# Kernel optimization log

Measured on AMD Instinct MI355X. Metric: run time of the kernel, lower is better.

## Reference

```python
import jax, jax.numpy as jnp
import numpy as np

T = 4          # spiking time steps
TAU = 2.0      # LIF leak
ALPHA = 4.0    # surrogate sigmoid sharpness
EPS = 1e-5     # batchnorm eps
HEADS = 12
SCALE = 0.125

@jax.custom_vjp
def spike(x):
    return (x >= 0).astype(x.dtype)

def _spike_fwd(x):
    return (x >= 0).astype(x.dtype), x

def _spike_bwd(x, g):
    s = jax.nn.sigmoid(ALPHA * x)
    return (g * ALPHA * s * (1.0 - s),)

spike.defvjp(_spike_fwd, _spike_bwd)

def lif(x, threshold):
    # x: (T*B, ...). layer_by_layer LIF: scan membrane over time axis.
    xt = x.reshape((T, -1) + x.shape[1:])
    def step(mem, xi):
        mem = mem + (xi - mem) / TAU
        s = spike(mem - threshold)
        mem = mem * (1.0 - jax.lax.stop_gradient(s))  # hard reset, detached
        return mem, s
    _, spikes = jax.lax.scan(step, jnp.zeros_like(xt[0]), xt)
    return spikes.reshape(x.shape)

def bn(x, gamma, beta):
    # training-mode batchnorm over all axes except channel axis 1
    axes = (0,) + tuple(range(2, x.ndim))
    mean = x.mean(axes, keepdims=True)
    var = x.var(axes, keepdims=True)
    shp = (1, -1) + (1,) * (x.ndim - 2)
    return (x - mean) * jax.lax.rsqrt(var + EPS) * gamma.reshape(shp) + beta.reshape(shp)

def forward(x, q_w, q_gamma, q_beta, k_w, k_gamma, k_beta, v_w, v_gamma, v_beta,
            proj_w, proj_b, proj_gamma, proj_beta,
            fc1_w, fc1_b, bn1_gamma, bn1_beta, fc2_w, fc2_b, bn2_gamma, bn2_beta):
    TB, C, H, W = x.shape
    N = H * W
    dh = C // HEADS
    xf = x.reshape(TB, C, N)

    def qkv_branch(w, g, b):
        y = lif(bn(jnp.einsum('oc,bcn->bon', w, xf), g, b), 1.0)  # (TB,C,N)
        # (TB,C,N) -> (TB,N,C) -> (TB,N,h,d) -> (TB,h,N,d)
        return y.transpose(0, 2, 1).reshape(TB, N, HEADS, dh).transpose(0, 2, 1, 3)

    q = qkv_branch(q_w, q_gamma, q_beta)
    k = qkv_branch(k_w, k_gamma, k_beta)
    v = qkv_branch(v_w, v_gamma, v_beta)

    kv = jnp.einsum('bhnd,bhne->bhde', k, v)          # (TB,h,d,d)
    attn = jnp.einsum('bhnd,bhde->bhne', q, kv) * SCALE  # (TB,h,N,d)
    attn = attn.transpose(0, 1, 3, 2)                 # (TB,h,d,N)
    attn = lif(attn, 0.5).reshape(TB, C, N)

    proj = jnp.einsum('oc,bcn->bon', proj_w, attn) + proj_b[None, :, None]
    proj = lif(bn(proj, proj_gamma, proj_beta), 1.0).reshape(TB, C, H, W)
    x = x + proj

    h1 = jnp.einsum('oc,bchw->bohw', fc1_w, x) + fc1_b.reshape(1, -1, 1, 1)
    h1 = lif(bn(h1, bn1_gamma, bn1_beta), 1.0)
    h2 = jnp.einsum('oc,bchw->bohw', fc2_w, h1) + fc2_b.reshape(1, -1, 1, 1)
    h2 = lif(bn(h2, bn2_gamma, bn2_beta), 1.0)
    return x + h2

def setup_inputs():
    key = jax.random.key(0)
    B, C, H, W = 32, 384, 14, 14
    Hd = 4 * C
    ks = jax.random.split(key, 8)
    sC = 1.0 / np.sqrt(C)
    sH = 1.0 / np.sqrt(Hd)
    return {
        'x': jax.random.normal(ks[0], (T * B, C, H, W), jnp.float32),
        'q_w': jax.random.normal(ks[1], (C, C), jnp.float32) * sC,
        'q_gamma': jnp.ones((C,), jnp.float32), 'q_beta': jnp.zeros((C,), jnp.float32),
        'k_w': jax.random.normal(ks[2], (C, C), jnp.float32) * sC,
        'k_gamma': jnp.ones((C,), jnp.float32), 'k_beta': jnp.zeros((C,), jnp.float32),
        'v_w': jax.random.normal(ks[3], (C, C), jnp.float32) * sC,
        'v_gamma': jnp.ones((C,), jnp.float32), 'v_beta': jnp.zeros((C,), jnp.float32),
        'proj_w': jax.random.normal(ks[4], (C, C), jnp.float32) * sC,
        'proj_b': jnp.zeros((C,), jnp.float32),
        'proj_gamma': jnp.ones((C,), jnp.float32), 'proj_beta': jnp.zeros((C,), jnp.float32),
        'fc1_w': jax.random.normal(ks[5], (Hd, C), jnp.float32) * sC,
        'fc1_b': jnp.zeros((Hd,), jnp.float32),
        'bn1_gamma': jnp.ones((Hd,), jnp.float32), 'bn1_beta': jnp.zeros((Hd,), jnp.float32),
        'fc2_w': jax.random.normal(ks[6], (C, Hd), jnp.float32) * sH,
        'fc2_b': jnp.zeros((C,), jnp.float32),
        'bn2_gamma': jnp.ones((C,), jnp.float32), 'bn2_beta': jnp.zeros((C,), jnp.float32),
    }

def reference(x, q_w, q_gamma, q_beta, k_w, k_gamma, k_beta, v_w, v_gamma, v_beta,
              proj_w, proj_b, proj_gamma, proj_beta,
              fc1_w, fc1_b, bn1_gamma, bn1_beta, fc2_w, fc2_b, bn2_gamma, bn2_beta):
    return forward(x, q_w, q_gamma, q_beta, k_w, k_gamma, k_beta, v_w, v_gamma, v_beta,
                   proj_w, proj_b, proj_gamma, proj_beta,
                   fc1_w, fc1_b, bn1_gamma, bn1_beta, fc2_w, fc2_b, bn2_gamma, bn2_beta)
```

## Files before the change

kernel.cpp:

```cpp
#include <hip/hip_runtime.h>
#include <stdint.h>

#define NBN   25088
#define NTOK  196
#define BATCH 32
#define CDIM  384
#define HDIM  1536
#define NHEAD 12

typedef float f32x4 __attribute__((ext_vector_type(4)));

#define GLDS16(g, l) __builtin_amdgcn_global_load_lds( \
    (const __attribute__((address_space(1))) void*)(g), \
    (__attribute__((address_space(3))) void*)(l), 16, 0, 0)

__global__ __launch_bounds__(256) void k_transpose(const float* __restrict__ x,
                                                   float* __restrict__ xT) {
  int id = blockIdx.x * 256 + threadIdx.x;
  int c = id / NBN;
  int r = id - c * NBN;
  int b = r / NTOK;
  int n = r - b * NTOK;
  xT[id] = x[((size_t)b * CDIM + c) * NTOK + n];
}

__global__ __launch_bounds__(256) void k_wT(const float* __restrict__ src,
                                            float* __restrict__ dst,
                                            int C, int ldd, int coff) {
  __shared__ float t[32][33];
  const int c0 = blockIdx.x * 32, r0 = blockIdx.y * 32;
  const int tx = threadIdx.x & 31, ty = threadIdx.x >> 5;
#pragma unroll
  for (int i = 0; i < 4; ++i)
    t[ty + i * 8][tx] = src[(size_t)(r0 + ty + i * 8) * C + c0 + tx];
  __syncthreads();
#pragma unroll
  for (int i = 0; i < 4; ++i)
    dst[(size_t)(c0 + ty + i * 8) * ldd + coff + r0 + tx] = t[tx][ty + i * 8];
}

template <typename TIN, int MT>
__global__ __launch_bounds__(256, 3) void k_gemm10(
    const float* __restrict__ WT, const TIN* __restrict__ X,
    const float* __restrict__ bias, float* __restrict__ Y,
    double* __restrict__ pS, double* __restrict__ pS2, int K, int Mtot) {
  __shared__ float As[32][MT];
  __shared__ float Bs[32][128];
  constexpr int MR = MT / 16;
  const int tid = threadIdx.x;
  const int lane = tid & 63, wv = tid >> 6;
  const int gy = blockIdx.x, bn = blockIdx.y;
  const int wcol = gy * MT;
  const int tx = tid & 15, ty = tid >> 4;
  const int NK = K >> 5;

  float acc[MR][8];
#pragma unroll
  for (int i = 0; i < MR; ++i)
#pragma unroll
    for (int j = 0; j < 8; ++j) acc[i][j] = 0.f;

  for (int ks = 0; ks < NK; ++ks) {
    const int k0 = ks << 5;
    __syncthreads();
    if constexpr (MT == 128) {
      const int lrow = wv * 2 + (lane >> 5), lcol = (lane & 31) * 4;
#pragma unroll
      for (int i = 0; i < 4; ++i)
        GLDS16(WT + (size_t)(k0 + i * 8 + lrow) * Mtot + wcol + lcol,
               &As[i * 8 + wv * 2][0]);
    } else {
      const int lrow = wv * 4 + (lane >> 4), lcol = (lane & 15) * 4;
#pragma unroll
      for (int i = 0; i < 2; ++i)
        GLDS16(WT + (size_t)(k0 + i * 16 + lrow) * Mtot + wcol + lcol,
               &As[i * 16 + wv * 4][0]);
    }
    if constexpr (__is_same(TIN, float)) {
      const int lrow = wv * 2 + (lane >> 5), lcol = (lane & 31) * 4;
#pragma unroll
      for (int i = 0; i < 4; ++i)
        GLDS16(X + (size_t)(k0 + i * 8 + lrow) * NBN + bn * 128 + lcol,
               &Bs[i * 8 + wv * 2][0]);
    } else {
      const int r = tid >> 3, c16 = tid & 7;
      const uint4 d = *reinterpret_cast<const uint4*>(
          &X[(size_t)(k0 + r) * NBN + bn * 128 + c16 * 16]);
      const uint32_t wd[4] = {d.x, d.y, d.z, d.w};
#pragma unroll
      for (int q = 0; q < 4; ++q) {
        f32x4 f;
        f[0] = (float)(wd[q] & 0xffu);
        f[1] = (float)((wd[q] >> 8) & 0xffu);
        f[2] = (float)((wd[q] >> 16) & 0xffu);
        f[3] = (float)(wd[q] >> 24);
        *reinterpret_cast<f32x4*>(&Bs[r][c16 * 16 + q * 4]) = f;
      }
    }
    asm volatile("s_waitcnt vmcnt(0)" ::: "memory");
    __syncthreads();

    auto lA0 = [&](int kk) { return *reinterpret_cast<const f32x4*>(&As[kk][ty * 4]); };
    auto lA1 = [&](int kk) { return *reinterpret_cast<const f32x4*>(&As[kk][64 + ty * 4]); };
    auto lB0 = [&](int kk) { return *reinterpret_cast<const f32x4*>(&Bs[kk][tx * 4]); };
    auto lB1 = [&](int kk) { return *reinterpret_cast<const f32x4*>(&Bs[kk][64 + tx * 4]); };
    auto FMA = [&](f32x4 a0, f32x4 a1, f32x4 b0, f32x4 b1) {
#pragma unroll
      for (int i = 0; i < MR; ++i) {
        const float av = (i < 4) ? a0[i] : a1[i - 4];
#pragma unroll
        for (int j = 0; j < 8; ++j) {
          const float bv = (j < 4) ? b0[j] : b1[j - 4];
          acc[i][j] = fmaf(av, bv, acc[i][j]);
        }
      }
    };
    f32x4 xa0, xa1, xb0, xb1, ya0, ya1, yb0, yb1;
    xa0 = lA0(0);
    if constexpr (MT == 128) xa1 = lA1(0);
    xb0 = lB0(0);
    xb1 = lB1(0);
#pragma unroll
    for (int kk = 0; kk < 32; kk += 2) {
      ya0 = lA0(kk + 1);
      if constexpr (MT == 128) ya1 = lA1(kk + 1);
      yb0 = lB0(kk + 1);
      yb1 = lB1(kk + 1);
      FMA(xa0, xa1, xb0, xb1);
      if (kk + 2 < 32) {
        xa0 = lA0(kk + 2);
        if constexpr (MT == 128) xa1 = lA1(kk + 2);
        xb0 = lB0(kk + 2);
        xb1 = lB1(kk + 2);
      }
      FMA(ya0, ya1, yb0, yb1);
    }
  }

#pragma unroll
  for (int i = 0; i < MR; ++i) {
    const int rl = (MT == 128) ? ((i < 4) ? (ty * 4 + i) : (64 + ty * 4 + i - 4))
                               : (ty * 4 + i);
    const int row = wcol + rl;
    const float bv = bias ? bias[row] : 0.f;
    float4 o0, o1;
    o0.x = acc[i][0] + bv; o0.y = acc[i][1] + bv;
    o0.z = acc[i][2] + bv; o0.w = acc[i][3] + bv;
    o1.x = acc[i][4] + bv; o1.y = acc[i][5] + bv;
    o1.z = acc[i][6] + bv; o1.w = acc[i][7] + bv;
    *reinterpret_cast<float4*>(&Y[(size_t)row * NBN + bn * 128 + tx * 4]) = o0;
    *reinterpret_cast<float4*>(&Y[(size_t)row * NBN + bn * 128 + 64 + tx * 4]) = o1;
    double s = (double)o0.x + (double)o0.y + (double)o0.z + (double)o0.w +
               (double)o1.x + (double)o1.y + (double)o1.z + (double)o1.w;
    double s2 = (double)o0.x * o0.x + (double)o0.y * o0.y + (double)o0.z * o0.z +
                (double)o0.w * o0.w + (double)o1.x * o1.x + (double)o1.y * o1.y +
                (double)o1.z * o1.z + (double)o1.w * o1.w;
#pragma unroll
    for (int off = 1; off < 16; off <<= 1) {
      s += __shfl_xor(s, off, 64);
      s2 += __shfl_xor(s2, off, 64);
    }
    if (tx == 0) {
      pS[(size_t)bn * Mtot + row] = s;
      pS2[(size_t)bn * Mtot + row] = s2;
    }
  }
}

__global__ __launch_bounds__(256) void k_repack(const uint8_t* __restrict__ sp,
                                                uint32_t* __restrict__ bitsT) {
  __shared__ uint32_t bb[64][48];
  const int col0 = blockIdx.x * 64;
  const int c = threadIdx.x & 63, q = threadIdx.x >> 6;
#pragma unroll
  for (int wi = 0; wi < 12; ++wi) {
    const int w = q * 12 + wi;
    uint32_t word = 0;
#pragma unroll
    for (int j = 0; j < 32; ++j)
      word |= (uint32_t)(sp[(size_t)(32 * w + j) * NBN + col0 + c] & 1) << j;
    bb[c][w] = word;
  }
  __syncthreads();
  for (int i = threadIdx.x; i < 64 * 48; i += 256)
    bitsT[(size_t)col0 * 48 + i] = bb[i / 48][i % 48];
}

__global__ __launch_bounds__(256) void k_spgemm(
    const uint32_t* __restrict__ bitsT, const float* __restrict__ WT,
    const float* __restrict__ bias, float* __restrict__ Y,
    double* __restrict__ pS, double* __restrict__ pS2) {
  __shared__ float ytile[4][384];
  const int tid = threadIdx.x;
  const int lane = tid & 63, wv = tid >> 6;
  const int c = blockIdx.x * 4 + wv;
  const uint32_t* wb = bitsT + (size_t)c * 48;

  float a0 = 0.f, a1 = 0.f, a2 = 0.f, a3 = 0.f, a4 = 0.f, a5 = 0.f;
  for (int w = 0; w < 48; ++w) {
    uint32_t word = wb[w];
    while (word) {
      const int k = w * 32 + __builtin_ctz(word);
      word &= word - 1;
      const float* wr = WT + (size_t)k * 384;
      a0 += wr[lane];
      a1 += wr[64 + lane];
      a2 += wr[128 + lane];
      a3 += wr[192 + lane];
      a4 += wr[256 + lane];
      a5 += wr[320 + lane];
    }
  }
  ytile[wv][lane]       = a0 + bias[lane];
  ytile[wv][64 + lane]  = a1 + bias[64 + lane];
  ytile[wv][128 + lane] = a2 + bias[128 + lane];
  ytile[wv][192 + lane] = a3 + bias[192 + lane];
  ytile[wv][256 + lane] = a4 + bias[256 + lane];
  ytile[wv][320 + lane] = a5 + bias[320 + lane];
  __syncthreads();
  const int c0 = blockIdx.x * 4;
  for (int r = tid; r < 384; r += 256) {
    float4 v;
    v.x = ytile[0][r]; v.y = ytile[1][r]; v.z = ytile[2][r]; v.w = ytile[3][r];
    *reinterpret_cast<float4*>(&Y[(size_t)r * NBN + c0]) = v;
    double s = (double)v.x + (double)v.y + (double)v.z + (double)v.w;
    double s2 = (double)v.x * v.x + (double)v.y * v.y + (double)v.z * v.z +
                (double)v.w * v.w;
    pS[(size_t)blockIdx.x * 384 + r] = s;
    pS2[(size_t)blockIdx.x * 384 + r] = s2;
  }
}

__global__ __launch_bounds__(64) void k_bn_reduceN(const double* __restrict__ pS,
                                                   const double* __restrict__ pS2,
                                                   float* __restrict__ mean,
                                                   float* __restrict__ rstd,
                                                   int Mtot, int NP) {
  const int ch = blockIdx.x, lane = threadIdx.x;
  double s = 0.0, s2 = 0.0;
  for (int j = lane; j < NP; j += 64) {
    s += pS[(size_t)j * Mtot + ch];
    s2 += pS2[(size_t)j * Mtot + ch];
  }
#pragma unroll
  for (int off = 32; off; off >>= 1) {
    s += __shfl_down(s, off, 64);
    s2 += __shfl_down(s2, off, 64);
  }
  if (lane == 0) {
    double m = s / (double)NBN;
    double v = s2 / (double)NBN - m * m;
    mean[ch] = (float)m;
    rstd[ch] = (float)(1.0 / sqrt(v + 1e-5));
  }
}

__global__ __launch_bounds__(256) void k_lif_pack(const float* __restrict__ Y,
    const float* __restrict__ mean, const float* __restrict__ rstd,
    const float* __restrict__ g0, const float* __restrict__ g1,
    const float* __restrict__ g2, const float* __restrict__ b0,
    const float* __restrict__ b1, const float* __restrict__ b2,
    uint32_t* __restrict__ pk) {
  const int o = blockIdx.x;
  const int b = threadIdx.x >> 3, w = threadIdx.x & 7;
  int br = o / 384, ol = o - br * 384;
  const float g = (br == 0 ? g0 : br == 1 ? g1 : g2)[ol];
  const float be = (br == 0 ? b0 : br == 1 ? b1 : b2)[ol];
  const float m_ = mean[o], rs_ = rstd[o];
  float mem[32];
#pragma unroll
  for (int j = 0; j < 32; ++j) mem[j] = 0.f;
  for (int t = 0; t < 4; ++t) {
    uint32_t word = 0;
    const size_t base = (size_t)o * NBN + (size_t)(t * 32 + b) * NTOK + w * 32;
#pragma unroll
    for (int q = 0; q < 8; ++q) {
      if (w * 32 + q * 4 < NTOK) {
        float4 v4 = *reinterpret_cast<const float4*>(&Y[base + q * 4]);
        float vv[4] = {v4.x, v4.y, v4.z, v4.w};
#pragma unroll
        for (int jj = 0; jj < 4; ++jj) {
          int j = q * 4 + jj;
          float v = ((vv[jj] - m_) * rs_) * g + be;
          float mm = mem[j];
          mm = mm + (v - mm) * 0.5f;
          bool fire = (mm >= 1.0f);
          mem[j] = fire ? 0.f : mm;
          word |= (fire ? 1u : 0u) << j;
        }
      }
    }
    pk[((size_t)o * 128 + t * 32 + b) * 8 + w] = word;
  }
}

__global__ __launch_bounds__(256) void k_lif_u8(const float* __restrict__ Y,
    const float* __restrict__ mean, const float* __restrict__ rstd,
    const float* __restrict__ gamma, const float* __restrict__ beta,
    uint8_t* __restrict__ sp) {
  const int o = blockIdx.x;
  const int b = threadIdx.x >> 3, w = threadIdx.x & 7;
  const float m_ = mean[o], rs_ = rstd[o], g = gamma[o], be = beta[o];
  float mem[32];
#pragma unroll
  for (int j = 0; j < 32; ++j) mem[j] = 0.f;
  for (int t = 0; t < 4; ++t) {
    const size_t base = (size_t)o * NBN + (size_t)(t * 32 + b) * NTOK + w * 32;
    uint32_t words[8];
#pragma unroll
    for (int q = 0; q < 8; ++q) {
      words[q] = 0;
      if (w * 32 + q * 4 < NTOK) {
        float4 v4 = *reinterpret_cast<const float4*>(&Y[base + q * 4]);
        float vv[4] = {v4.x, v4.y, v4.z, v4.w};
#pragma unroll
        for (int jj = 0; jj < 4; ++jj) {
          int j = q * 4 + jj;
          float v = ((vv[jj] - m_) * rs_) * g + be;
          float mm = mem[j];
          mm = mm + (v - mm) * 0.5f;
          bool fire = (mm >= 1.0f);
          mem[j] = fire ? 0.f : mm;
          words[q] |= (fire ? 1u : 0u) << (8 * jj);
        }
      }
    }
    uint32_t* dst = reinterpret_cast<uint32_t*>(const_cast<uint8_t*>(sp) + base);
#pragma unroll
    for (int q = 0; q < 8; ++q)
      if (w * 32 + q * 4 < NTOK) dst[q] = words[q];
  }
}

template <int MODE>
__global__ __launch_bounds__(256) void k_bn_lif(const float* __restrict__ Y,
                                                const float* __restrict__ mean,
                                                const float* __restrict__ rstd,
                                                const float* __restrict__ gamma,
                                                const float* __restrict__ beta,
                                                const float* __restrict__ addsrc,
                                                float* __restrict__ extra) {
  int id = blockIdx.x * 256 + threadIdx.x;
  int o = id / (BATCH * NTOK);
  int r = id - o * (BATCH * NTOK);
  float m_ = mean[o], rs_ = rstd[o], g = gamma[o], be = beta[o];
  float mem = 0.f;
#pragma unroll
  for (int t = 0; t < 4; ++t) {
    size_t idx = (size_t)o * NBN + (size_t)t * (BATCH * NTOK) + r;
    float v = Y[idx];
    v = ((v - m_) * rs_) * g + be;
    mem = mem + (v - mem) * 0.5f;
    bool fire = (mem >= 1.0f);
    float s = fire ? 1.f : 0.f;
    mem = fire ? 0.f : mem;
    if constexpr (MODE == 1) {
      extra[idx] = addsrc[idx] + s;
    } else {
      int b = r / NTOK, n = r - b * NTOK;
      extra[((size_t)(t * BATCH + b) * CDIM + o) * NTOK + n] = addsrc[idx] + s;
    }
  }
}

__global__ __launch_bounds__(256) void k_attn_pop(const uint32_t* __restrict__ pQ,
                                                  const uint32_t* __restrict__ pK,
                                                  const uint32_t* __restrict__ pV,
                                                  uint8_t* __restrict__ spA) {
  __shared__ __align__(16) uint32_t qw[32][8], kw[32][8], vw[32][8];
  __shared__ int kv[32][33];
  __shared__ uint32_t kvb[8][32];
  __shared__ uint32_t qT[NTOK];
  const int bh = blockIdx.x;
  const int b_ = bh / NHEAD, h = bh - b_ * NHEAD;
  const int tid = threadIdx.x;
  const int e = tid >> 3, w = tid & 7;
  float mem[32];
#pragma unroll
  for (int j = 0; j < 32; ++j) mem[j] = 0.f;

  for (int t = 0; t < 4; ++t) {
    const int tb = t * 32 + b_;
    {
      int d = tid >> 3, wo = tid & 7;
      size_t base = ((size_t)(h * 32 + d) * 128 + tb) * 8 + wo;
      qw[d][wo] = pQ[base];
      kw[d][wo] = pK[base];
      vw[d][wo] = pV[base];
    }
    __syncthreads();
    for (int i = tid; i < 1024; i += 256) {
      int d = i >> 5, ee = i & 31;
      const uint64_t* kp = reinterpret_cast<const uint64_t*>(&kw[d][0]);
      const uint64_t* vp = reinterpret_cast<const uint64_t*>(&vw[ee][0]);
      int s = 0;
#pragma unroll
      for (int u = 0; u < 4; ++u) s += __popcll(kp[u] & vp[u]);
      kv[d][ee] = s;
    }
    __syncthreads();
    {
      int bitb = tid >> 5, ee = tid & 31;
      uint32_t mword = 0;
#pragma unroll
      for (int d = 0; d < 32; ++d) mword |= (uint32_t)((kv[d][ee] >> bitb) & 1) << d;
      kvb[bitb][ee] = mword;
    }
    if (tid < NTOK) {
      uint32_t mword = 0;
#pragma unroll
      for (int d = 0; d < 32; ++d)
        mword |= ((qw[d][tid >> 5] >> (tid & 31)) & 1u) << d;
      qT[tid] = mword;
    }
    __syncthreads();
    uint32_t word = 0;
#pragma unroll
    for (int j = 0; j < 32; ++j) {
      int n = w * 32 + j;
      if (n < NTOK) {
        uint32_t qm = qT[n];
        int acc = 0;
#pragma unroll
        for (int bb = 0; bb < 8; ++bb) acc += __popc(qm & kvb[bb][e]) << bb;
        float val = (float)acc * 0.125f;
        float mm = mem[j];
        mm = mm + (val - mm) * 0.5f;
        bool fire = (mm >= 0.5f);
        mem[j] = fire ? 0.f : mm;
        word |= (fire ? 1u : 0u) << j;
      }
    }
    uint8_t* dst = spA + (size_t)(h * 32 + e) * NBN + (size_t)tb * NTOK + w * 32;
#pragma unroll
    for (int q = 0; q < 8; ++q) {
      if (w * 32 + q * 4 < NTOK) {
        uint32_t b4 = ((word >> (q * 4)) & 1u) | (((word >> (q * 4 + 1)) & 1u) << 8) |
                      (((word >> (q * 4 + 2)) & 1u) << 16) |
                      (((word >> (q * 4 + 3)) & 1u) << 24);
        *reinterpret_cast<uint32_t*>(dst + q * 4) = b4;
      }
    }
    __syncthreads();
  }
}

extern "C" void kernel_launch(void* const* d_in, const int* in_sizes, int n_in,
                              void* d_out, int out_size, void* d_ws, size_t ws_size,
                              hipStream_t stream) {
  const float* x          = (const float*)d_in[0];
  const float* q_w        = (const float*)d_in[1];
  const float* q_gamma    = (const float*)d_in[2];
  const float* q_beta     = (const float*)d_in[3];
  const float* k_w        = (const float*)d_in[4];
  const float* k_gamma    = (const float*)d_in[5];
  const float* k_beta     = (const float*)d_in[6];
  const float* v_w        = (const float*)d_in[7];
  const float* v_gamma    = (const float*)d_in[8];
  const float* v_beta     = (const float*)d_in[9];
  const float* proj_w     = (const float*)d_in[10];
  const float* proj_b     = (const float*)d_in[11];
  const float* proj_gamma = (const float*)d_in[12];
  const float* proj_beta  = (const float*)d_in[13];
  const float* fc1_w      = (const float*)d_in[14];
  const float* fc1_b      = (const float*)d_in[15];
  const float* bn1_gamma  = (const float*)d_in[16];
  const float* bn1_beta   = (const float*)d_in[17];
  const float* fc2_w      = (const float*)d_in[18];
  const float* fc2_b      = (const float*)d_in[19];
  const float* bn2_gamma  = (const float*)d_in[20];
  const float* bn2_beta   = (const float*)d_in[21];
  float* out = (float*)d_out;
  char* ws = (char*)d_ws;

  const size_t O_XT   = 0;
  const size_t O_YQ   = 38535168;
  const size_t O_XRES = 154140672;
  const size_t O_PK   = 192675840;
  const size_t O_SPA  = 197394432;
  const size_t O_H1SP = 192675840;
  const size_t O_H1   = 0;
  const size_t O_ST   = 231211008;
  const size_t O_P1   = 154140672;
  const size_t O_P1B  = O_P1 + 1806336;
  const size_t O_QKVT = 197394432;
  const size_t O_PRJT = 192675840;
  const size_t O_P2A  = 192675840;
  const size_t O_P2AB = O_P2A + 2408448;
  const size_t O_F1T  = 197492736;
  const size_t O_BT   = 0;
  const size_t O_F2T  = 4816896;
  const size_t O_P2B  = 77070336;
  const size_t O_P2BB = 96337920;

  float* xT    = (float*)(ws + O_XT);
  float* yQ    = (float*)(ws + O_YQ);
  float* yB    = (float*)(ws + O_YQ);
  float* h1    = (float*)(ws + O_H1);
  float* xres  = (float*)(ws + O_XRES);
  uint32_t* pkQKV = (uint32_t*)(ws + O_PK);
  uint8_t* spA   = (uint8_t*)(ws + O_SPA);
  uint8_t* h1sp  = (uint8_t*)(ws + O_H1SP);
  float* qkvT  = (float*)(ws + O_QKVT);
  float* projT = (float*)(ws + O_PRJT);
  float* fc1T  = (float*)(ws + O_F1T);
  float* fc2T  = (float*)(ws + O_F2T);
  uint32_t* bitsT = (uint32_t*)(ws + O_BT);
  double* p1S  = (double*)(ws + O_P1);
  double* p1S2 = (double*)(ws + O_P1B);
  double* p2aS  = (double*)(ws + O_P2A);
  double* p2aS2 = (double*)(ws + O_P2AB);
  double* p2bS  = (double*)(ws + O_P2B);
  double* p2bS2 = (double*)(ws + O_P2BB);
  float* mean_ = (float*)(ws + O_ST);
  float* rstd_ = (float*)(ws + O_ST + 6144);

  k_transpose<<<dim3(CDIM * NBN / 256), 256, 0, stream>>>(x, xT);
  k_wT<<<dim3(12, 12), 256, 0, stream>>>(q_w, qkvT, 384, 1152, 0);
  k_wT<<<dim3(12, 12), 256, 0, stream>>>(k_w, qkvT, 384, 1152, 384);
  k_wT<<<dim3(12, 12), 256, 0, stream>>>(v_w, qkvT, 384, 1152, 768);

  k_gemm10<float, 128><<<dim3(9, 196), 256, 0, stream>>>(
      qkvT, xT, (const float*)nullptr, yQ, p1S, p1S2, CDIM, 1152);
  k_bn_reduceN<<<dim3(1152), 64, 0, stream>>>(p1S, p1S2, mean_, rstd_, 1152, 196);
  k_lif_pack<<<dim3(1152), 256, 0, stream>>>(
      yQ, mean_, rstd_, q_gamma, k_gamma, v_gamma, q_beta, k_beta, v_beta, pkQKV);

  k_attn_pop<<<dim3(BATCH * NHEAD), 256, 0, stream>>>(
      pkQKV, pkQKV + 393216, pkQKV + 786432, spA);

  k_wT<<<dim3(12, 12), 256, 0, stream>>>(proj_w, projT, 384, 384, 0);
  k_gemm10<uint8_t, 64><<<dim3(6, 196), 256, 0, stream>>>(
      projT, spA, proj_b, yB, p1S, p1S2, CDIM, 384);
  k_bn_reduceN<<<dim3(384), 64, 0, stream>>>(p1S, p1S2, mean_, rstd_, 384, 196);
  k_bn_lif<1><<<dim3(9408), 256, 0, stream>>>(yB, mean_, rstd_, proj_gamma, proj_beta,
                                              xT, xres);

  k_wT<<<dim3(12, 48), 256, 0, stream>>>(fc1_w, fc1T, 384, 1536, 0);
  k_gemm10<float, 128><<<dim3(12, 196), 256, 0, stream>>>(
      fc1T, xres, fc1_b, h1, p2aS, p2aS2, CDIM, 1536);
  k_bn_reduceN<<<dim3(1536), 64, 0, stream>>>(p2aS, p2aS2, mean_, rstd_, 1536, 196);
  k_lif_u8<<<dim3(1536), 256, 0, stream>>>(h1, mean_, rstd_,
                                           bn1_gamma, bn1_beta, h1sp);

  k_wT<<<dim3(48, 12), 256, 0, stream>>>(fc2_w, fc2T, 1536, 384, 0);
  k_repack<<<dim3(NBN / 64), 256, 0, stream>>>(h1sp, bitsT);
  k_spgemm<<<dim3(NBN / 4), 256, 0, stream>>>(bitsT, fc2T, fc2_b, yB, p2bS, p2bS2);
  k_bn_reduceN<<<dim3(384), 64, 0, stream>>>(p2bS, p2bS2, mean_, rstd_, 384, NBN / 4);
  k_bn_lif<2><<<dim3(9408), 256, 0, stream>>>(yB, mean_, rstd_, bn2_gamma, bn2_beta,
                                              xres, out);
}
```

Before: 1.098 ms.

## Fuse fc1 LIF with bit repack and remap GEMM workgroups across XCDs

```diff
diff --git a/kernel.cpp b/kernel.cpp
--- a/kernel.cpp
+++ b/kernel.cpp
@@ -43,13 +43,20 @@
 __global__ __launch_bounds__(256, 3) void k_gemm10(
     const float* __restrict__ WT, const TIN* __restrict__ X,
     const float* __restrict__ bias, float* __restrict__ Y,
-    double* __restrict__ pS, double* __restrict__ pS2, int K, int Mtot) {
+    double* __restrict__ pS, double* __restrict__ pS2, int K, int Mtot, int ngy) {
   __shared__ float As[32][MT];
   __shared__ float Bs[32][128];
   constexpr int MR = MT / 16;
   const int tid = threadIdx.x;
   const int lane = tid & 63, wv = tid >> 6;
-  const int gy = blockIdx.x, bn = blockIdx.y;
+  const int nwg = gridDim.x;
+  const int lid = blockIdx.x;
+  const int xcd = lid & 7, pos = lid >> 3;
+  const int q8 = nwg >> 3, rem = nwg & 7;
+  const int wgid = (xcd < rem ? xcd * (q8 + 1)
+                              : rem * (q8 + 1) + (xcd - rem) * q8) + pos;
+  const int bn = wgid / ngy;
+  const int gy = wgid - bn * ngy;
   const int wcol = gy * MT;
   const int tx = tid & 15, ty = tid >> 4;
   const int NK = K >> 5;
@@ -167,23 +174,39 @@
   }
 }
 
-__global__ __launch_bounds__(256) void k_repack(const uint8_t* __restrict__ sp,
-                                                uint32_t* __restrict__ bitsT) {
-  __shared__ uint32_t bb[64][48];
-  const int col0 = blockIdx.x * 64;
-  const int c = threadIdx.x & 63, q = threadIdx.x >> 6;
-#pragma unroll
-  for (int wi = 0; wi < 12; ++wi) {
-    const int w = q * 12 + wi;
+__global__ __launch_bounds__(128) void k_lif_bits(const float* __restrict__ Y,
+    const float* __restrict__ mean, const float* __restrict__ rstd,
+    const float* __restrict__ gamma, const float* __restrict__ beta,
+    uint32_t* __restrict__ bitsT) {
+  __shared__ float sm[32], sr[32], sg[32], sb[32];
+  const int cb = blockIdx.x;
+  const int w = blockIdx.y;
+  const int tid = threadIdx.x;
+  if (tid < 32) {
+    const int ch = w * 32 + tid;
+    sm[tid] = mean[ch]; sr[tid] = rstd[ch];
+    sg[tid] = gamma[ch]; sb[tid] = beta[ch];
+  }
+  __syncthreads();
+  const int r = cb * 128 + tid;
+  float mem[32];
+#pragma unroll
+  for (int j = 0; j < 32; ++j) mem[j] = 0.f;
+  for (int t = 0; t < 4; ++t) {
     uint32_t word = 0;
 #pragma unroll
-    for (int j = 0; j < 32; ++j)
-      word |= (uint32_t)(sp[(size_t)(32 * w + j) * NBN + col0 + c] & 1) << j;
-    bb[c][w] = word;
-  }
-  __syncthreads();
-  for (int i = threadIdx.x; i < 64 * 48; i += 256)
-    bitsT[(size_t)col0 * 48 + i] = bb[i / 48][i % 48];
+    for (int j = 0; j < 32; ++j) {
+      const int ch = w * 32 + j;
+      float v = Y[(size_t)ch * NBN + t * (BATCH * NTOK) + r];
+      v = ((v - sm[j]) * sr[j]) * sg[j] + sb[j];
+      float mm = mem[j];
+      mm = mm + (v - mm) * 0.5f;
+      bool fire = (mm >= 1.0f);
+      mem[j] = fire ? 0.f : mm;
+      word |= (fire ? 1u : 0u) << j;
+    }
+    bitsT[(size_t)(t * (BATCH * NTOK) + r) * 48 + w] = word;
+  }
 }
 
 __global__ __launch_bounds__(256) void k_spgemm(
@@ -291,44 +314,6 @@
       }
     }
     pk[((size_t)o * 128 + t * 32 + b) * 8 + w] = word;
-  }
-}
-
-__global__ __launch_bounds__(256) void k_lif_u8(const float* __restrict__ Y,
-    const float* __restrict__ mean, const float* __restrict__ rstd,
-    const float* __restrict__ gamma, const float* __restrict__ beta,
-    uint8_t* __restrict__ sp) {
-  const int o = blockIdx.x;
-  const int b = threadIdx.x >> 3, w = threadIdx.x & 7;
-  const float m_ = mean[o], rs_ = rstd[o], g = gamma[o], be = beta[o];
-  float mem[32];
-#pragma unroll
-  for (int j = 0; j < 32; ++j) mem[j] = 0.f;
-  for (int t = 0; t < 4; ++t) {
-    const size_t base = (size_t)o * NBN + (size_t)(t * 32 + b) * NTOK + w * 32;
-    uint32_t words[8];
-#pragma unroll
-    for (int q = 0; q < 8; ++q) {
-      words[q] = 0;
-      if (w * 32 + q * 4 < NTOK) {
-        float4 v4 = *reinterpret_cast<const float4*>(&Y[base + q * 4]);
-        float vv[4] = {v4.x, v4.y, v4.z, v4.w};
-#pragma unroll
-        for (int jj = 0; jj < 4; ++jj) {
-          int j = q * 4 + jj;
-          float v = ((vv[jj] - m_) * rs_) * g + be;
-          float mm = mem[j];
-          mm = mm + (v - mm) * 0.5f;
-          bool fire = (mm >= 1.0f);
-          mem[j] = fire ? 0.f : mm;
-          words[q] |= (fire ? 1u : 0u) << (8 * jj);
-        }
-      }
-    }
-    uint32_t* dst = reinterpret_cast<uint32_t*>(const_cast<uint8_t*>(sp) + base);
-#pragma unroll
-    for (int q = 0; q < 8; ++q)
-      if (w * 32 + q * 4 < NTOK) dst[q] = words[q];
   }
 }
 
@@ -478,7 +463,6 @@
   const size_t O_XRES = 154140672;
   const size_t O_PK   = 192675840;
   const size_t O_SPA  = 197394432;
-  const size_t O_H1SP = 192675840;
   const size_t O_H1   = 0;
   const size_t O_ST   = 231211008;
   const size_t O_P1   = 154140672;
@@ -488,7 +472,7 @@
   const size_t O_P2A  = 192675840;
   const size_t O_P2AB = O_P2A + 2408448;
   const size_t O_F1T  = 197492736;
-  const size_t O_BT   = 0;
+  const size_t O_BT   = 192675840;
   const size_t O_F2T  = 4816896;
   const size_t O_P2B  = 77070336;
   const size_t O_P2BB = 96337920;
@@ -500,7 +484,6 @@
   float* xres  = (float*)(ws + O_XRES);
   uint32_t* pkQKV = (uint32_t*)(ws + O_PK);
   uint8_t* spA   = (uint8_t*)(ws + O_SPA);
-  uint8_t* h1sp  = (uint8_t*)(ws + O_H1SP);
   float* qkvT  = (float*)(ws + O_QKVT);
   float* projT = (float*)(ws + O_PRJT);
   float* fc1T  = (float*)(ws + O_F1T);
@@ -520,8 +503,8 @@
   k_wT<<<dim3(12, 12), 256, 0, stream>>>(k_w, qkvT, 384, 1152, 384);
   k_wT<<<dim3(12, 12), 256, 0, stream>>>(v_w, qkvT, 384, 1152, 768);
 
-  k_gemm10<float, 128><<<dim3(9, 196), 256, 0, stream>>>(
-      qkvT, xT, (const float*)nullptr, yQ, p1S, p1S2, CDIM, 1152);
+  k_gemm10<float, 128><<<dim3(9 * 196), 256, 0, stream>>>(
+      qkvT, xT, (const float*)nullptr, yQ, p1S, p1S2, CDIM, 1152, 9);
   k_bn_reduceN<<<dim3(1152), 64, 0, stream>>>(p1S, p1S2, mean_, rstd_, 1152, 196);
   k_lif_pack<<<dim3(1152), 256, 0, stream>>>(
       yQ, mean_, rstd_, q_gamma, k_gamma, v_gamma, q_beta, k_beta, v_beta, pkQKV);
@@ -530,21 +513,20 @@
       pkQKV, pkQKV + 393216, pkQKV + 786432, spA);
 
   k_wT<<<dim3(12, 12), 256, 0, stream>>>(proj_w, projT, 384, 384, 0);
-  k_gemm10<uint8_t, 64><<<dim3(6, 196), 256, 0, stream>>>(
-      projT, spA, proj_b, yB, p1S, p1S2, CDIM, 384);
+  k_gemm10<uint8_t, 64><<<dim3(6 * 196), 256, 0, stream>>>(
+      projT, spA, proj_b, yB, p1S, p1S2, CDIM, 384, 6);
   k_bn_reduceN<<<dim3(384), 64, 0, stream>>>(p1S, p1S2, mean_, rstd_, 384, 196);
   k_bn_lif<1><<<dim3(9408), 256, 0, stream>>>(yB, mean_, rstd_, proj_gamma, proj_beta,
                                               xT, xres);
 
   k_wT<<<dim3(12, 48), 256, 0, stream>>>(fc1_w, fc1T, 384, 1536, 0);
-  k_gemm10<float, 128><<<dim3(12, 196), 256, 0, stream>>>(
-      fc1T, xres, fc1_b, h1, p2aS, p2aS2, CDIM, 1536);
+  k_gemm10<float, 128><<<dim3(12 * 196), 256, 0, stream>>>(
+      fc1T, xres, fc1_b, h1, p2aS, p2aS2, CDIM, 1536, 12);
   k_bn_reduceN<<<dim3(1536), 64, 0, stream>>>(p2aS, p2aS2, mean_, rstd_, 1536, 196);
-  k_lif_u8<<<dim3(1536), 256, 0, stream>>>(h1, mean_, rstd_,
-                                           bn1_gamma, bn1_beta, h1sp);
+  k_lif_bits<<<dim3(49, 48), 128, 0, stream>>>(h1, mean_, rstd_,
+                                               bn1_gamma, bn1_beta, bitsT);
 
   k_wT<<<dim3(48, 12), 256, 0, stream>>>(fc2_w, fc2T, 1536, 384, 0);
-  k_repack<<<dim3(NBN / 64), 256, 0, stream>>>(h1sp, bitsT);
   k_spgemm<<<dim3(NBN / 4), 256, 0, stream>>>(bitsT, fc2T, fc2_b, yB, p2bS, p2bS2);
   k_bn_reduceN<<<dim3(384), 64, 0, stream>>>(p2bS, p2bS2, mean_, rstd_, 384, NBN / 4);
   k_bn_lif<2><<<dim3(9408), 256, 0, stream>>>(yB, mean_, rstd_, bn2_gamma, bn2_beta,
```

After: 1.035 ms, median of 2. 5.7% less time.
